# Kernel optimization log

Hardware: AMD Instinct MI355X
Metric: run time of the kernel (lower is better)

Reference implementation:

```python
import jax, jax.numpy as jnp
import numpy as np

N = 50000
E = 800000
IN_C = 128
HID = 128
OUT_C = 128
EPS = 1e-5


def _glorot(key, shape):
    fan_in = shape[-1]
    return jax.random.normal(key, shape, dtype=jnp.float32) / jnp.sqrt(jnp.float32(fan_in))


def setup_inputs() -> dict:
    key = jax.random.key(0)
    ks = jax.random.split(key, 16)
    inp = {
        'x': jax.random.normal(ks[0], (N, IN_C), dtype=jnp.float32),
        'edge_index': jax.random.randint(ks[1], (2, E), 0, N, dtype=jnp.int64),
    }
    dims = [(IN_C, HID), (HID, HID), (HID, OUT_C)]
    for i, (din, dout) in enumerate(dims, start=1):
        inp[f'Wl{i}'] = _glorot(ks[2 * i], (dout, din))      # applied to aggregated neighbors
        inp[f'bl{i}'] = jnp.zeros((dout,), dtype=jnp.float32)
        inp[f'Wr{i}'] = _glorot(ks[2 * i + 1], (dout, din))  # applied to root node
        inp[f'g{i}'] = jnp.ones((dout,), dtype=jnp.float32)   # BN gamma
        inp[f'b{i}'] = jnp.zeros((dout,), dtype=jnp.float32)  # BN beta
    inp['Wlin'] = _glorot(ks[10], (OUT_C, 2 * HID + OUT_C))
    inp['blin'] = jnp.zeros((OUT_C,), dtype=jnp.float32)
    return inp


def _sage(x, src, dst, Wl, bl, Wr):
    # mean aggregation of source features at target nodes (PyG SAGEConv default)
    msg = x[src]                                              # [E, C]
    s = jax.ops.segment_sum(msg, dst, num_segments=N)         # [N, C]
    cnt = jax.ops.segment_sum(jnp.ones((src.shape[0], 1), x.dtype), dst, num_segments=N)
    aggr = s / jnp.maximum(cnt, 1.0)
    return aggr @ Wl.T + bl + x @ Wr.T


def _bn(x, g, b):
    # training-mode BatchNorm1d over the node dimension
    mu = jnp.mean(x, axis=0)
    var = jnp.var(x, axis=0)
    return g * (x - mu) * jax.lax.rsqrt(var + EPS) + b


def reference(x, edge_index, Wl1, bl1, Wr1, g1, b1, Wl2, bl2, Wr2, g2, b2,
              Wl3, bl3, Wr3, g3, b3, Wlin, blin):
    src, dst = edge_index[0], edge_index[1]
    x1 = _bn(jax.nn.relu(_sage(x, src, dst, Wl1, bl1, Wr1)), g1, b1)
    x2 = _bn(jax.nn.relu(_sage(x1, src, dst, Wl2, bl2, Wr2)), g2, b2)
    x3 = _bn(jax.nn.relu(_sage(x2, src, dst, Wl3, bl3, Wr3)), g3, b3)
    cat = jnp.concatenate([x1, x2, x3], axis=-1)              # [N, 2*HID + OUT_C]
    return jax.nn.relu(cat @ Wlin.T + blin)
```

## Files before the change

### kernel.cpp

```cpp
#include <hip/hip_runtime.h>

#define NN 50000
#define NE 800000
#define CH 128
#define EPSV 1e-5f

typedef unsigned short ushort_t;
typedef __attribute__((ext_vector_type(8))) short short8_t;
typedef __attribute__((ext_vector_type(8))) unsigned short u16x8;
typedef __attribute__((ext_vector_type(4))) float f32x4;

__device__ inline float bf2f(ushort_t u) {
    union { unsigned int i; float f; } t; t.i = ((unsigned int)u) << 16; return t.f;
}
__device__ inline ushort_t f2bf(float f) {
    union { float f; unsigned int i; } t; t.f = f;
    unsigned int r = t.i + 0x7fff + ((t.i >> 16) & 1);
    return (ushort_t)(r >> 16);
}


__global__ void k_hist(const int* __restrict__ dst, int* __restrict__ deg) {
    int e = blockIdx.x * blockDim.x + threadIdx.x;
    if (e < NE) atomicAdd(&deg[dst[e]], 1);
}

__global__ void k_scan(const int* __restrict__ deg, int* __restrict__ row_ptr) {
    __shared__ int wsum[16];
    const int t = threadIdx.x;
    const int lane = t & 63;
    const int wid = t >> 6;
    int carry = 0;
    for (int base = 0; base < NN; base += 1024) {
        int i = base + t;
        int v = (i < NN) ? deg[i] : 0;
        int x = v;
        #pragma unroll
        for (int off = 1; off < 64; off <<= 1) {
            int y = __shfl_up(x, off, 64);
            if (lane >= off) x += y;
        }
        if (lane == 63) wsum[wid] = x;
        __syncthreads();
        if (wid == 0 && lane < 16) {
            int s = wsum[lane];
            #pragma unroll
            for (int off = 1; off < 16; off <<= 1) {
                int y = __shfl_up(s, off, 16);
                if (lane >= off) s += y;
            }
            wsum[lane] = s;
        }
        __syncthreads();
        int wbase = (wid > 0) ? wsum[wid - 1] : 0;
        if (i < NN) row_ptr[i] = carry + wbase + x - v;
        carry += wsum[15];
        __syncthreads();
    }
    if (t == 0) row_ptr[NN] = carry;
}

__global__ void k_fill(const int* __restrict__ src, const int* __restrict__ dst,
                       const int* __restrict__ row_ptr, int* __restrict__ fillc,
                       int* __restrict__ csr) {
    int e = blockIdx.x * blockDim.x + threadIdx.x;
    if (e < NE) {
        int d = dst[e];
        int pos = row_ptr[d] + atomicAdd(&fillc[d], 1);
        csr[pos] = src[e];
    }
}


__global__ __launch_bounds__(256) void k_cvtX(const float* __restrict__ x,
                                              ushort_t* __restrict__ xb) {
    int i = blockIdx.x * 256 + threadIdx.x;
    if (i >= NN * 32) return;
    float4 v = ((const float4*)x)[i];
    ushort4 o;
    o.x = f2bf(v.x); o.y = f2bf(v.y); o.z = f2bf(v.z); o.w = f2bf(v.w);
    ((ushort4*)xb)[i] = o;
}

__global__ __launch_bounds__(256) void k_pack2(const float* __restrict__ s0,
                                               const float* __restrict__ s1,
                                               ushort_t* __restrict__ dst) {
    int t = blockIdx.x * 256 + threadIdx.x;
    if (t >= 128 * 256) return;
    int o = t >> 8, k = t & 255;
    float v = (k < 128) ? s0[o * 128 + k] : s1[o * 128 + k - 128];
    dst[t] = f2bf(v);
}

__global__ void k_packfold(const float* __restrict__ Wl, const float* __restrict__ Wr,
                           const float* __restrict__ ab, const float* __restrict__ bl,
                           ushort_t* __restrict__ Wp, float* __restrict__ bias) {
    __shared__ float red[128];
    int o = blockIdx.x;
    int k = threadIdx.x;
    float wr = Wr[o * 128 + k];
    Wp[o * 256 + k]       = f2bf(Wl[o * 128 + k]);
    Wp[o * 256 + 128 + k] = f2bf(wr * ab[k]);
    red[k] = wr * ab[128 + k];
    __syncthreads();
    for (int s = 64; s > 0; s >>= 1) {
        if (k < s) red[k] += red[k + s];
        __syncthreads();
    }
    if (k == 0) bias[o] = bl[o] + red[0];
}

__global__ void k_packfoldF(const float* __restrict__ Wlin,
                            const float* __restrict__ ab1, const float* __restrict__ ab2,
                            const float* __restrict__ ab3, const float* __restrict__ blin,
                            ushort_t* __restrict__ Wp, float* __restrict__ bias) {
    __shared__ float red[128];
    int o = blockIdx.x;
    int k = threadIdx.x;
    const float* abs_[3] = {ab1, ab2, ab3};
    float dot = 0.f;
    #pragma unroll
    for (int i = 0; i < 3; ++i) {
        float w = Wlin[o * 384 + i * 128 + k];
        Wp[o * 384 + i * 128 + k] = f2bf(w * abs_[i][k]);
        dot += w * abs_[i][128 + k];
    }
    red[k] = dot;
    __syncthreads();
    for (int s = 64; s > 0; s >>= 1) {
        if (k < s) red[k] += red[k + s];
        __syncthreads();
    }
    if (k == 0) bias[o] = blin[o] + red[0];
}


template<bool FOLD>
__global__ __launch_bounds__(256) void k_aggr(const ushort_t* __restrict__ x,
        const int* __restrict__ row_ptr, const int* __restrict__ csr,
        const float* __restrict__ ab, ushort_t* __restrict__ aggr) {
    const int node = blockIdx.x * 4 + (threadIdx.x >> 6);
    const int lane = threadIdx.x & 63;
    const int l4 = lane & 15;
    const int q  = lane >> 4;
    const int r0 = row_ptr[node], r1 = row_ptr[node + 1];
    const int d = r1 - r0;

    float accA[8] = {0, 0, 0, 0, 0, 0, 0, 0};
    float accB[8] = {0, 0, 0, 0, 0, 0, 0, 0};

    int j = r0 + q;
    for (; j + 4 < r1; j += 8) {
        int s0 = csr[j], s1 = csr[j + 4];
        u16x8 v0 = *(const u16x8*)&x[(size_t)s0 * CH + l4 * 8];
        u16x8 v1 = *(const u16x8*)&x[(size_t)s1 * CH + l4 * 8];
        #pragma unroll
        for (int i = 0; i < 8; ++i) {
            accA[i] += bf2f(v0[i]);
            accB[i] += bf2f(v1[i]);
        }
    }
    for (; j < r1; j += 4) {
        int s0 = csr[j];
        u16x8 v0 = *(const u16x8*)&x[(size_t)s0 * CH + l4 * 8];
        #pragma unroll
        for (int i = 0; i < 8; ++i) accA[i] += bf2f(v0[i]);
    }

    const float sc = d > 0 ? 1.0f / (float)d : 0.0f;
    #pragma unroll
    for (int i = 0; i < 8; ++i) {
        float s = accA[i] + accB[i];
        s += __shfl_xor(s, 16);
        s += __shfl_xor(s, 32);
        accA[i] = s * sc;
    }

    if (q == 0) {
        u16x8 ov;
        #pragma unroll
        for (int i = 0; i < 8; ++i) {
            float v = accA[i];
            if (FOLD) v = d > 0 ? fmaf(v, ab[l4 * 8 + i], ab[128 + l4 * 8 + i]) : 0.f;
            ov[i] = f2bf(v);
        }
        *(u16x8*)&aggr[(size_t)node * CH + l4 * 8] = ov;
    }
}


#define STAGE(buf, t) do {                                                           \
    const ushort_t* Ab_ = (((t) >> 1) == 0) ? A0 : ((((t) >> 1) == 1) ? A1 : A2);    \
    Ab_ += ((t) & 1) * 64;                                                           \
    const ushort_t* Wb_ = W + (t) * 64;                                              \
    _Pragma("unroll")                                                                \
    for (int i_ = 0; i_ < 4; ++i_) {                                                 \
        int f_ = i_ * 256 + tid;                                                     \
        int row_ = f_ >> 3;                                                          \
        int c_ = (f_ & 7) ^ (row_ & 7);                                              \
        int gr_ = bn0 + row_; gr_ = gr_ < NN ? gr_ : NN - 1;                         \
        __builtin_amdgcn_global_load_lds(                                            \
            (const __attribute__((address_space(1))) unsigned int*)(Ab_ + (size_t)gr_ * CH + c_ * 8), \
            (__attribute__((address_space(3))) unsigned int*)(&Abuf[buf][f_ * 8]),   \
            16, 0, 0);                                                               \
        __builtin_amdgcn_global_load_lds(                                            \
            (const __attribute__((address_space(1))) unsigned int*)(Wb_ + (size_t)row_ * (NT * 64) + c_ * 8), \
            (__attribute__((address_space(3))) unsigned int*)(&Wbuf[buf][f_ * 8]),   \
            16, 0, 0);                                                               \
    } } while (0)

template<int NT, bool STATS, bool F32OUT>
__global__ __launch_bounds__(256, 2) void k_mgemm(
    const ushort_t* __restrict__ A0, const ushort_t* __restrict__ A1,
    const ushort_t* __restrict__ A2,
    const ushort_t* __restrict__ W, const float* __restrict__ bias,
    ushort_t* __restrict__ outb, float* __restrict__ outf,
    float* __restrict__ bn_sums)
{
    __shared__ __align__(16) ushort_t Abuf[2][128 * 64];
    __shared__ __align__(16) ushort_t Wbuf[2][128 * 64];
    __shared__ float bns[128], bnq[128];

    const int tid  = threadIdx.x;
    const int lane = tid & 63;
    const int wid  = tid >> 6;
    const int l15  = lane & 15;
    const int lg   = lane >> 4;
    const int wn   = (wid >> 1) * 64;
    const int wo   = (wid & 1) * 64;
    const int bn0  = blockIdx.x * 128;

    if (STATS && tid < 128) { bns[tid] = 0.f; bnq[tid] = 0.f; }

    f32x4 acc[4][4];
    #pragma unroll
    for (int i = 0; i < 4; ++i)
        #pragma unroll
        for (int j = 0; j < 4; ++j)
            acc[i][j] = (f32x4){0.f, 0.f, 0.f, 0.f};

    STAGE(0, 0);
    asm volatile("s_waitcnt vmcnt(0)");
    __syncthreads();

    #pragma unroll
    for (int t = 0; t < NT; ++t) {
        const int cur = t & 1;
        if (t + 1 < NT) STAGE(cur ^ 1, t + 1);
        #pragma unroll
        for (int s = 0; s < 2; ++s) {
            short8_t af[4], wf[4];
            #pragma unroll
            for (int b = 0; b < 4; ++b) {
                int ra = wn + b * 16 + l15;
                int ca = (s * 4 + lg) ^ (ra & 7);
                af[b] = *(const short8_t*)&Abuf[cur][ra * 64 + ca * 8];
                int rw = wo + b * 16 + l15;
                int cw = (s * 4 + lg) ^ (rw & 7);
                wf[b] = *(const short8_t*)&Wbuf[cur][rw * 64 + cw * 8];
            }
            #pragma unroll
            for (int i = 0; i < 4; ++i)
                #pragma unroll
                for (int j = 0; j < 4; ++j)
                    acc[i][j] = __builtin_amdgcn_mfma_f32_16x16x32_bf16(
                        af[i], wf[j], acc[i][j], 0, 0, 0);
        }
        asm volatile("s_waitcnt vmcnt(0)");
        __syncthreads();
    }

    float bv[4];
    #pragma unroll
    for (int j = 0; j < 4; ++j) bv[j] = bias[wo + j * 16 + l15];

    float sum[4] = {0.f, 0.f, 0.f, 0.f}, sq[4] = {0.f, 0.f, 0.f, 0.f};

    #pragma unroll
    for (int i = 0; i < 4; ++i) {
        #pragma unroll
        for (int r = 0; r < 4; ++r) {
            int gn = bn0 + wn + i * 16 + lg * 4 + r;
            bool ok = gn < NN;
            #pragma unroll
            for (int j = 0; j < 4; ++j) {
                int o = wo + j * 16 + l15;
                float v = acc[i][j][r] + bv[j];
                v = fmaxf(v, 0.f);
                if (ok) {
                    if (F32OUT) outf[(size_t)gn * CH + o] = v;
                    else        outb[(size_t)gn * CH + o] = f2bf(v);
                    if (STATS) { sum[j] += v; sq[j] += v * v; }
                }
            }
        }
    }

    if (STATS) {
        #pragma unroll
        for (int j = 0; j < 4; ++j) {
            float ss = sum[j], qq = sq[j];
            ss += __shfl_xor(ss, 16); qq += __shfl_xor(qq, 16);
            ss += __shfl_xor(ss, 32); qq += __shfl_xor(qq, 32);
            if (lg == 0) {
                atomicAdd(&bns[wo + j * 16 + l15], ss);
                atomicAdd(&bnq[wo + j * 16 + l15], qq);
            }
        }
        __syncthreads();
        if (tid < 128) {
            atomicAdd(&bn_sums[tid], bns[tid]);
            atomicAdd(&bn_sums[128 + tid], bnq[tid]);
        }
    }
}


__global__ void k_bnfin(const float* __restrict__ bn_sums, const float* __restrict__ g,
                        const float* __restrict__ b, float* __restrict__ ab) {
    int o = threadIdx.x;
    float mu = bn_sums[o] * (1.0f / NN);
    float var = bn_sums[128 + o] * (1.0f / NN) - mu * mu;
    var = var > 0.f ? var : 0.f;
    float rstd = rsqrtf(var + EPSV);
    float a = g[o] * rstd;
    ab[o] = a;
    ab[128 + o] = b[o] - a * mu;
}


extern "C" void kernel_launch(void* const* d_in, const int* in_sizes, int n_in,
                              void* d_out, int out_size, void* d_ws, size_t ws_size,
                              hipStream_t stream) {
    const float* x  = (const float*)d_in[0];
    const int*   ei = (const int*)d_in[1];
    const int* esrc = ei;
    const int* edst = ei + NE;

    const float* Wl[3] = {(const float*)d_in[2],  (const float*)d_in[7],  (const float*)d_in[12]};
    const float* bl[3] = {(const float*)d_in[3],  (const float*)d_in[8],  (const float*)d_in[13]};
    const float* Wr[3] = {(const float*)d_in[4],  (const float*)d_in[9],  (const float*)d_in[14]};
    const float* gg[3] = {(const float*)d_in[5],  (const float*)d_in[10], (const float*)d_in[15]};
    const float* bb[3] = {(const float*)d_in[6],  (const float*)d_in[11], (const float*)d_in[16]};
    const float* Wlin  = (const float*)d_in[17];
    const float* blin  = (const float*)d_in[18];

    float* fo = (float*)d_out;

    const size_t NC = (size_t)NN * CH;
    ushort_t* xb     = (ushort_t*)d_ws;
    ushort_t* y1b    = xb + NC;
    ushort_t* y2b    = y1b + NC;
    ushort_t* y3b    = y2b + NC;
    ushort_t* aggr_b = y3b + NC;
    ushort_t* Wp1    = aggr_b + NC;
    ushort_t* Wp2    = Wp1 + 128 * 256;
    ushort_t* Wp3    = Wp2 + 128 * 256;
    ushort_t* WpF    = Wp3 + 128 * 256;
    float* bias2     = (float*)(WpF + 128 * 384);
    float* bias3     = bias2 + 128;
    float* biasF     = bias3 + 128;
    float* bn_sums   = biasF + 128;
    float* ab        = bn_sums + 768;
    int* row_ptr     = (int*)(ab + 768);
    int* fillc       = row_ptr + NN + 1;
    int* csr         = fillc + NN;

    hipMemsetAsync(fillc, 0, NN * sizeof(int), stream);
    k_hist<<<(NE + 255) / 256, 256, 0, stream>>>(edst, fillc);
    k_scan<<<1, 1024, 0, stream>>>(fillc, row_ptr);
    hipMemsetAsync(fillc, 0, NN * sizeof(int), stream);
    k_fill<<<(NE + 255) / 256, 256, 0, stream>>>(esrc, edst, row_ptr, fillc, csr);

    k_cvtX<<<(NN * 32 + 255) / 256, 256, 0, stream>>>(x, xb);
    k_pack2<<<128, 256, 0, stream>>>(Wl[0], Wr[0], Wp1);
    hipMemsetAsync(bn_sums, 0, 768 * sizeof(float), stream);

    const int GEMM_GRID = (NN + 127) / 128;

    k_aggr<false><<<NN / 4, 256, 0, stream>>>(xb, row_ptr, csr, nullptr, aggr_b);
    k_mgemm<4, true, false><<<GEMM_GRID, 256, 0, stream>>>(
        aggr_b, xb, nullptr, Wp1, bl[0], y1b, nullptr, bn_sums);
    k_bnfin<<<1, 128, 0, stream>>>(bn_sums, gg[0], bb[0], ab);
    k_packfold<<<128, 128, 0, stream>>>(Wl[1], Wr[1], ab, bl[1], Wp2, bias2);

    k_aggr<true><<<NN / 4, 256, 0, stream>>>(y1b, row_ptr, csr, ab, aggr_b);
    k_mgemm<4, true, false><<<GEMM_GRID, 256, 0, stream>>>(
        aggr_b, y1b, nullptr, Wp2, bias2, y2b, nullptr, bn_sums + 256);
    k_bnfin<<<1, 128, 0, stream>>>(bn_sums + 256, gg[1], bb[1], ab + 256);
    k_packfold<<<128, 128, 0, stream>>>(Wl[2], Wr[2], ab + 256, bl[2], Wp3, bias3);

    k_aggr<true><<<NN / 4, 256, 0, stream>>>(y2b, row_ptr, csr, ab + 256, aggr_b);
    k_mgemm<4, true, false><<<GEMM_GRID, 256, 0, stream>>>(
        aggr_b, y2b, nullptr, Wp3, bias3, y3b, nullptr, bn_sums + 512);
    k_bnfin<<<1, 128, 0, stream>>>(bn_sums + 512, gg[2], bb[2], ab + 512);
    k_packfoldF<<<128, 128, 0, stream>>>(Wlin, ab, ab + 256, ab + 512, blin, WpF, biasF);

    k_mgemm<6, false, true><<<GEMM_GRID, 256, 0, stream>>>(
        y1b, y2b, y3b, WpF, biasF, nullptr, fo, nullptr);
}
```

Baseline: 373.3 us.

## Fuse BN finalize into fold kernels, drop memsets, split CSR fill by range

The BN finalize step is folded into the weight-folding kernels, so the separate k_bnfin launches go away. The scan now zeroes the degree counters and cvtX zeroes the BN sums, which removes two memsets. The CSR fill is split into two passes over destination ranges, meant to improve atomic and scatter locality. The aggregation loop is unrolled to four neighbor loads per iteration for more memory-level parallelism. In exchange, the edge list is read twice during the fill and every fold block recomputes the BN statistics.

```diff
diff --git a/kernel.cpp b/kernel.cpp
--- a/kernel.cpp
+++ b/kernel.cpp
@@ -4,6 +4,8 @@
 #define NE 800000
 #define CH 128
 #define EPSV 1e-5f
+#define NPASS 2
+#define PRANGE 25000
 
 typedef unsigned short ushort_t;
 typedef __attribute__((ext_vector_type(8))) short short8_t;
@@ -21,11 +23,11 @@
 
 
 __global__ void k_hist(const int* __restrict__ dst, int* __restrict__ deg) {
-    int e = blockIdx.x * blockDim.x + threadIdx.x;
+    int e = blockIdx.x * 256 + threadIdx.x;
     if (e < NE) atomicAdd(&deg[dst[e]], 1);
 }
 
-__global__ void k_scan(const int* __restrict__ deg, int* __restrict__ row_ptr) {
+__global__ void k_scan(int* __restrict__ deg, int* __restrict__ row_ptr) {
     __shared__ int wsum[16];
     const int t = threadIdx.x;
     const int lane = t & 63;
@@ -34,6 +36,7 @@
     for (int base = 0; base < NN; base += 1024) {
         int i = base + t;
         int v = (i < NN) ? deg[i] : 0;
+        if (i < NN) deg[i] = 0;
         int x = v;
         #pragma unroll
         for (int off = 1; off < 64; off <<= 1) {
@@ -60,21 +63,30 @@
     if (t == 0) row_ptr[NN] = carry;
 }
 
-__global__ void k_fill(const int* __restrict__ src, const int* __restrict__ dst,
-                       const int* __restrict__ row_ptr, int* __restrict__ fillc,
-                       int* __restrict__ csr) {
-    int e = blockIdx.x * blockDim.x + threadIdx.x;
+__global__ void k_fillp(const int* __restrict__ src, const int* __restrict__ dst,
+                        const int* __restrict__ row_ptr, int* __restrict__ fillc,
+                        int* __restrict__ csr, int lo, int hi) {
+    int e = blockIdx.x * 256 + threadIdx.x;
     if (e < NE) {
         int d = dst[e];
-        int pos = row_ptr[d] + atomicAdd(&fillc[d], 1);
-        csr[pos] = src[e];
+        int s = src[e];
+        if (d >= lo && d < hi) {
+            int pos = row_ptr[d] + atomicAdd(&fillc[d], 1);
+            csr[pos] = s;
+        }
     }
 }
 
 
 __global__ __launch_bounds__(256) void k_cvtX(const float* __restrict__ x,
-                                              ushort_t* __restrict__ xb) {
+                                              ushort_t* __restrict__ xb,
+                                              float* __restrict__ bn_sums) {
     int i = blockIdx.x * 256 + threadIdx.x;
+    if (blockIdx.x == 0) {
+        bn_sums[threadIdx.x] = 0.f;
+        bn_sums[256 + threadIdx.x] = 0.f;
+        bn_sums[512 + threadIdx.x] = 0.f;
+    }
     if (i >= NN * 32) return;
     float4 v = ((const float4*)x)[i];
     ushort4 o;
@@ -92,16 +104,25 @@
     dst[t] = f2bf(v);
 }
 
-__global__ void k_packfold(const float* __restrict__ Wl, const float* __restrict__ Wr,
-                           const float* __restrict__ ab, const float* __restrict__ bl,
-                           ushort_t* __restrict__ Wp, float* __restrict__ bias) {
+__global__ void k_foldnext(const float* __restrict__ bn_sums,
+                           const float* __restrict__ g, const float* __restrict__ b,
+                           const float* __restrict__ Wl, const float* __restrict__ Wr,
+                           const float* __restrict__ bl,
+                           ushort_t* __restrict__ Wp, float* __restrict__ bias,
+                           float* __restrict__ abg) {
     __shared__ float red[128];
     int o = blockIdx.x;
     int k = threadIdx.x;
+    float mu = bn_sums[k] * (1.0f / NN);
+    float var = bn_sums[128 + k] * (1.0f / NN) - mu * mu;
+    var = var > 0.f ? var : 0.f;
+    float a = g[k] * rsqrtf(var + EPSV);
+    float c = b[k] - a * mu;
+    if (o == 0) { abg[k] = a; abg[128 + k] = c; }
     float wr = Wr[o * 128 + k];
     Wp[o * 256 + k]       = f2bf(Wl[o * 128 + k]);
-    Wp[o * 256 + 128 + k] = f2bf(wr * ab[k]);
-    red[k] = wr * ab[128 + k];
+    Wp[o * 256 + 128 + k] = f2bf(wr * a);
+    red[k] = wr * c;
     __syncthreads();
     for (int s = 64; s > 0; s >>= 1) {
         if (k < s) red[k] += red[k + s];
@@ -110,22 +131,26 @@
     if (k == 0) bias[o] = bl[o] + red[0];
 }
 
-__global__ void k_packfoldF(const float* __restrict__ Wlin,
-                            const float* __restrict__ ab1, const float* __restrict__ ab2,
-                            const float* __restrict__ ab3, const float* __restrict__ blin,
-                            ushort_t* __restrict__ Wp, float* __restrict__ bias) {
+__global__ void k_foldF(const float* __restrict__ bn3,
+                        const float* __restrict__ g3, const float* __restrict__ b3,
+                        const float* __restrict__ ab1, const float* __restrict__ ab2,
+                        const float* __restrict__ Wlin, const float* __restrict__ blin,
+                        ushort_t* __restrict__ Wp, float* __restrict__ bias) {
     __shared__ float red[128];
     int o = blockIdx.x;
     int k = threadIdx.x;
-    const float* abs_[3] = {ab1, ab2, ab3};
-    float dot = 0.f;
-    #pragma unroll
-    for (int i = 0; i < 3; ++i) {
-        float w = Wlin[o * 384 + i * 128 + k];
-        Wp[o * 384 + i * 128 + k] = f2bf(w * abs_[i][k]);
-        dot += w * abs_[i][128 + k];
-    }
-    red[k] = dot;
+    float mu = bn3[k] * (1.0f / NN);
+    float var = bn3[128 + k] * (1.0f / NN) - mu * mu;
+    var = var > 0.f ? var : 0.f;
+    float a3 = g3[k] * rsqrtf(var + EPSV);
+    float c3 = b3[k] - a3 * mu;
+    float w1 = Wlin[o * 384 + k];
+    float w2 = Wlin[o * 384 + 128 + k];
+    float w3 = Wlin[o * 384 + 256 + k];
+    Wp[o * 384 + k]       = f2bf(w1 * ab1[k]);
+    Wp[o * 384 + 128 + k] = f2bf(w2 * ab2[k]);
+    Wp[o * 384 + 256 + k] = f2bf(w3 * a3);
+    red[k] = w1 * ab1[128 + k] + w2 * ab2[128 + k] + w3 * c3;
     __syncthreads();
     for (int s = 64; s > 0; s >>= 1) {
         if (k < s) red[k] += red[k + s];
@@ -145,24 +170,27 @@
     const int q  = lane >> 4;
     const int r0 = row_ptr[node], r1 = row_ptr[node + 1];
     const int d = r1 - r0;
+    const ushort_t* xrow = x + l4 * 8;
 
     float accA[8] = {0, 0, 0, 0, 0, 0, 0, 0};
     float accB[8] = {0, 0, 0, 0, 0, 0, 0, 0};
 
     int j = r0 + q;
-    for (; j + 4 < r1; j += 8) {
-        int s0 = csr[j], s1 = csr[j + 4];
-        u16x8 v0 = *(const u16x8*)&x[(size_t)s0 * CH + l4 * 8];
-        u16x8 v1 = *(const u16x8*)&x[(size_t)s1 * CH + l4 * 8];
+    for (; j + 12 < r1; j += 16) {
+        int s0 = csr[j], s1 = csr[j + 4], s2 = csr[j + 8], s3 = csr[j + 12];
+        u16x8 v0 = *(const u16x8*)(xrow + (size_t)s0 * CH);
+        u16x8 v1 = *(const u16x8*)(xrow + (size_t)s1 * CH);
+        u16x8 v2 = *(const u16x8*)(xrow + (size_t)s2 * CH);
+        u16x8 v3 = *(const u16x8*)(xrow + (size_t)s3 * CH);
         #pragma unroll
         for (int i = 0; i < 8; ++i) {
-            accA[i] += bf2f(v0[i]);
-            accB[i] += bf2f(v1[i]);
+            accA[i] += bf2f(v0[i]) + bf2f(v1[i]);
+            accB[i] += bf2f(v2[i]) + bf2f(v3[i]);
         }
     }
     for (; j < r1; j += 4) {
         int s0 = csr[j];
-        u16x8 v0 = *(const u16x8*)&x[(size_t)s0 * CH + l4 * 8];
+        u16x8 v0 = *(const u16x8*)(xrow + (size_t)s0 * CH);
         #pragma unroll
         for (int i = 0; i < 8; ++i) accA[i] += bf2f(v0[i]);
     }
@@ -316,19 +344,6 @@
 }
 
 
-__global__ void k_bnfin(const float* __restrict__ bn_sums, const float* __restrict__ g,
-                        const float* __restrict__ b, float* __restrict__ ab) {
-    int o = threadIdx.x;
-    float mu = bn_sums[o] * (1.0f / NN);
-    float var = bn_sums[128 + o] * (1.0f / NN) - mu * mu;
-    var = var > 0.f ? var : 0.f;
-    float rstd = rsqrtf(var + EPSV);
-    float a = g[o] * rstd;
-    ab[o] = a;
-    ab[128 + o] = b[o] - a * mu;
-}
-
-
 extern "C" void kernel_launch(void* const* d_in, const int* in_sizes, int n_in,
                               void* d_out, int out_size, void* d_ws, size_t ws_size,
                               hipStream_t stream) {
@@ -362,39 +377,39 @@
     float* biasF     = bias3 + 128;
     float* bn_sums   = biasF + 128;
     float* ab        = bn_sums + 768;
-    int* row_ptr     = (int*)(ab + 768);
+    int* row_ptr     = (int*)(ab + 512);
     int* fillc       = row_ptr + NN + 1;
     int* csr         = fillc + NN;
 
     hipMemsetAsync(fillc, 0, NN * sizeof(int), stream);
     k_hist<<<(NE + 255) / 256, 256, 0, stream>>>(edst, fillc);
     k_scan<<<1, 1024, 0, stream>>>(fillc, row_ptr);
-    hipMemsetAsync(fillc, 0, NN * sizeof(int), stream);
-    k_fill<<<(NE + 255) / 256, 256, 0, stream>>>(esrc, edst, row_ptr, fillc, csr);
-
-    k_cvtX<<<(NN * 32 + 255) / 256, 256, 0, stream>>>(x, xb);
+    for (int p = 0; p < NPASS; ++p)
+        k_fillp<<<NE / 256, 256, 0, stream>>>(esrc, edst, row_ptr, fillc, csr,
+                                              p * PRANGE, (p + 1) * PRANGE);
+
+    k_cvtX<<<(NN * 32 + 255) / 256, 256, 0, stream>>>(x, xb, bn_sums);
     k_pack2<<<128, 256, 0, stream>>>(Wl[0], Wr[0], Wp1);
-    hipMemsetAsync(bn_sums, 0, 768 * sizeof(float), stream);
 
     const int GEMM_GRID = (NN + 127) / 128;
 
     k_aggr<false><<<NN / 4, 256, 0, stream>>>(xb, row_ptr, csr, nullptr, aggr_b);
     k_mgemm<4, true, false><<<GEMM_GRID, 256, 0, stream>>>(
         aggr_b, xb, nullptr, Wp1, bl[0], y1b, nullptr, bn_sums);
-    k_bnfin<<<1, 128, 0, stream>>>(bn_sums, gg[0], bb[0], ab);
-    k_packfold<<<128, 128, 0, stream>>>(Wl[1], Wr[1], ab, bl[1], Wp2, bias2);
+    k_foldnext<<<128, 128, 0, stream>>>(bn_sums, gg[0], bb[0],
+                                        Wl[1], Wr[1], bl[1], Wp2, bias2, ab);
 
     k_aggr<true><<<NN / 4, 256, 0, stream>>>(y1b, row_ptr, csr, ab, aggr_b);
     k_mgemm<4, true, false><<<GEMM_GRID, 256, 0, stream>>>(
         aggr_b, y1b, nullptr, Wp2, bias2, y2b, nullptr, bn_sums + 256);
-    k_bnfin<<<1, 128, 0, stream>>>(bn_sums + 256, gg[1], bb[1], ab + 256);
-    k_packfold<<<128, 128, 0, stream>>>(Wl[2], Wr[2], ab + 256, bl[2], Wp3, bias3);
+    k_foldnext<<<128, 128, 0, stream>>>(bn_sums + 256, gg[1], bb[1],
+                                        Wl[2], Wr[2], bl[2], Wp3, bias3, ab + 256);
 
     k_aggr<true><<<NN / 4, 256, 0, stream>>>(y2b, row_ptr, csr, ab + 256, aggr_b);
     k_mgemm<4, true, false><<<GEMM_GRID, 256, 0, stream>>>(
         aggr_b, y2b, nullptr, Wp3, bias3, y3b, nullptr, bn_sums + 512);
-    k_bnfin<<<1, 128, 0, stream>>>(bn_sums + 512, gg[2], bb[2], ab + 512);
-    k_packfoldF<<<128, 128, 0, stream>>>(Wlin, ab, ab + 256, ab + 512, blin, WpF, biasF);
+    k_foldF<<<128, 128, 0, stream>>>(bn_sums + 512, gg[2], bb[2], ab, ab + 256,
+                                     Wlin, blin, WpF, biasF);
 
     k_mgemm<6, false, true><<<GEMM_GRID, 256, 0, stream>>>(
         y1b, y2b, y3b, WpF, biasF, nullptr, fo, nullptr);
```

Result: faster. 362.7 us (-2.8%).
